# Kernel tuning notes

Measured on AMD Instinct MI355X. Metric: run time of the kernel, lower is better.

## Reference

```python
import jax, jax.numpy as jnp
import numpy as np

B, N1, N2, E = 8, 32, 32, 256
H = 8                 # num_heads == args.vir_heads
KD = E // H           # key dim per head = 32
HD = E // H           # head dim (value_dim == embed_dim)
L = N1 * N2           # 1024 tokens
SCALING = KD ** -0.5
LN_EPS = 1e-5


def _rel_pos_2d():
    # RetNetRelPosDeform2D with zero offsets (vir_use_deformable=False)
    half = 1.0 / 10000.0 ** jnp.linspace(0.0, 1.0, KD // 2)
    angle = jnp.repeat(half, 2)                                   # (KD,) interleaved pairs
    decay = jnp.log(1.0 - 2.0 ** (-2.0 - 5.0 * jnp.arange(H, dtype=jnp.float32) / H))  # (H,)
    i1 = jnp.arange(N1, dtype=jnp.float32)
    i2 = jnp.arange(N2, dtype=jnp.float32)
    index_k = (i1[:, None] + i2[None, :]).reshape(L)              # (L,)
    sin_k = jnp.sin(index_k[:, None] * angle[None, :])            # (L, KD)
    cos_k = jnp.cos(index_k[:, None] * angle[None, :])
    # zero offsets => index_q == index_k, broadcast over (B, H)
    sin_q = sin_k[None, None]                                     # (1,1,L,KD)
    cos_q = cos_k[None, None]
    # Manhattan distance decay mask on the 2D grid
    d = (jnp.abs(i1[:, None, None, None] - i1[None, None, :, None])
         + jnp.abs(i2[None, :, None, None] - i2[None, None, None, :])).reshape(L, L)
    mask = jnp.exp(d[None, :, :] * decay[:, None, None])          # (H, L, L)
    mask = jnp.nan_to_num(mask)
    mask = mask / jnp.sqrt(mask.sum(-1, keepdims=True))
    return sin_q, cos_q, sin_k, cos_k, mask


def rotate_every_two(x):
    x1 = x[..., ::2]
    x2 = x[..., 1::2]
    return jnp.stack((-x2, x1), axis=-1).reshape(x.shape)


def theta_shift(x, sin, cos):
    return x * cos + rotate_every_two(x) * sin


def setup_inputs() -> dict:
    key = jax.random.key(0)
    ks = jax.random.split(key, 5)
    gain_qkv = 2.0 ** -2.5 * (6.0 / (E + E)) ** 0.5  # xavier_uniform bound scale
    gain_o = 2.0 ** -1 * (6.0 / (E + E)) ** 0.5
    x = jax.random.normal(ks[0], (B, N1, N2, E), dtype=jnp.float32)
    Wq = jax.random.uniform(ks[1], (E, E), jnp.float32, -gain_qkv, gain_qkv)
    Wk = jax.random.uniform(ks[2], (E, E), jnp.float32, -gain_qkv, gain_qkv)
    Wv = jax.random.uniform(ks[3], (E, E), jnp.float32, -gain_qkv, gain_qkv)
    Wo = jax.random.uniform(ks[4], (E, E), jnp.float32, -gain_o, gain_o)
    ln_g = jnp.ones((HD,), jnp.float32)
    ln_b = jnp.zeros((HD,), jnp.float32)
    return {"x": x, "Wq": Wq, "Wk": Wk, "Wv": Wv, "Wo": Wo, "ln_g": ln_g, "ln_b": ln_b}


def reference(x, Wq, Wk, Wv, Wo, ln_g, ln_b):
    sin_q, cos_q, sin_k, cos_k, mask = _rel_pos_2d()
    xf = x.reshape(B, L, E)
    q = (xf @ Wq.T).reshape(B, L, H, KD).transpose(0, 2, 1, 3)    # (B,H,L,KD)
    k = (xf @ Wk.T * SCALING).reshape(B, L, H, KD).transpose(0, 2, 1, 3)
    vr = (xf @ Wv.T).reshape(B, L, H, HD).transpose(0, 2, 1, 3)   # (B,H,L,HD)
    qr = theta_shift(q, sin_q, cos_q)
    kr = theta_shift(k, sin_k[None, None], cos_k[None, None])
    qk = jnp.einsum('bhqd,bhkd->bhqk', qr, kr) * mask[None]       # (B,H,L,L)
    den = jnp.clip(jax.lax.stop_gradient(jnp.abs(qk)).sum(-1, keepdims=True), 1.0, 5e4)
    qk = qk / den
    out = jnp.einsum('bhqk,bhkd->bhqd', qk, vr).transpose(0, 2, 1, 3)  # (B,L,H,HD)
    mu = out.mean(-1, keepdims=True)
    var = out.var(-1, keepdims=True)
    out = (out - mu) / jnp.sqrt(var + LN_EPS) * ln_g + ln_b       # per-head LayerNorm
    out = jax.nn.gelu(out.reshape(B, L, H * HD), approximate=False)
    out = out @ Wo.T
    return out.reshape(B, N1, N2, E)
```

## Files before the change

### kernel.cpp

```cpp
#include <hip/hip_runtime.h>
#include <math.h>

typedef unsigned short u16;
typedef unsigned int u32;
typedef __bf16 bf16x8 __attribute__((ext_vector_type(8)));
typedef float f32x4 __attribute__((ext_vector_type(4)));

#define SCALING 0.17677669529663687f
#define LOG2E 1.44269504088896f
#define LOG2_10000 13.287712379549449f

__device__ __forceinline__ u16 f2bf(float f) {
    u32 u; __builtin_memcpy(&u, &f, 4);
    u = u + 0x7FFFu + ((u >> 16) & 1u);
    return (u16)(u >> 16);
}
__device__ __forceinline__ f32x4 mfma16(bf16x8 a, bf16x8 b, f32x4 c) {
    return __builtin_amdgcn_mfma_f32_16x16x32_bf16(a, b, c, 0, 0, 0);
}
__device__ __forceinline__ float decay_l2(int h) {
    return logf(1.0f - exp2f(-2.0f - 0.625f * (float)h)) * LOG2E;
}

__global__ __launch_bounds__(256) void cvt_kernel(
    const float* __restrict__ x,
    const float* __restrict__ Wq, const float* __restrict__ Wk,
    const float* __restrict__ Wv, const float* __restrict__ Wo,
    u16* __restrict__ xb, u16* __restrict__ wb) {
    int bid = blockIdx.x;
    const float* src; u16* dst; int off;
    if (bid < 1024) { src = x; dst = xb; off = bid * 2048; }
    else {
        int wsel = (bid - 1024) >> 5;
        src = (wsel == 0) ? Wq : (wsel == 1) ? Wk : (wsel == 2) ? Wv : Wo;
        dst = wb + wsel * 65536;
        off = ((bid - 1024) & 31) * 2048;
    }
    int i = off + threadIdx.x * 8;
    float4 a = *(const float4*)&src[i];
    float4 b = *(const float4*)&src[i + 4];
    union { int4 v; u16 s[8]; } t;
    t.s[0] = f2bf(a.x); t.s[1] = f2bf(a.y); t.s[2] = f2bf(a.z); t.s[3] = f2bf(a.w);
    t.s[4] = f2bf(b.x); t.s[5] = f2bf(b.y); t.s[6] = f2bf(b.z); t.s[7] = f2bf(b.w);
    *(int4*)&dst[i] = t.v;
}

__global__ __launch_bounds__(256) void gemm_bt_kernel(
    const u16* __restrict__ A, const u16* __restrict__ Wb,
    u16* __restrict__ O0, u16* __restrict__ O1, u16* __restrict__ O2,
    float* __restrict__ Of, int mode_base) {
    __shared__ u16 As[64 * 136];
    __shared__ u16 Ws[64 * 136];
    int z = blockIdx.z;
    const u16* W = Wb + z * 65536;
    u16* O = (z == 0) ? O0 : (z == 1) ? O1 : O2;
    int mode = mode_base + z;
    int n0 = blockIdx.x * 64, r0 = blockIdx.y * 64;
    int tid = threadIdx.x;
    int w = tid >> 6, lane = tid & 63, ln = lane & 15, quad = lane >> 4;
    f32x4 acc[4] = {};
#pragma unroll
    for (int ch = 0; ch < 2; ch++) {
        int k0 = ch * 128;
        if (ch) __syncthreads();
#pragma unroll
        for (int i = 0; i < 4; i++) {
            int c = tid + i * 256;
            int row = c >> 4, seg = c & 15;
            *(int4*)&As[row * 136 + seg * 8] = *(const int4*)&A[(long)(r0 + row) * 256 + k0 + seg * 8];
            *(int4*)&Ws[row * 136 + seg * 8] = *(const int4*)&W[(long)(n0 + row) * 256 + k0 + seg * 8];
        }
        __syncthreads();
#pragma unroll
        for (int kt = 0; kt < 4; kt++) {
            bf16x8 a = *(const bf16x8*)&As[(w * 16 + ln) * 136 + kt * 32 + quad * 8];
#pragma unroll
            for (int nt = 0; nt < 4; nt++) {
                bf16x8 b = *(const bf16x8*)&Ws[(nt * 16 + ln) * 136 + kt * 32 + quad * 8];
                acc[nt] = mfma16(a, b, acc[nt]);
            }
        }
    }
    int rowg = r0 + w * 16 + quad * 4;
    if (mode == 3) {
#pragma unroll
        for (int nt = 0; nt < 4; nt++) {
            int e = n0 + nt * 16 + ln;
#pragma unroll
            for (int r = 0; r < 4; r++)
                Of[(long)(rowg + r) * 256 + e] = acc[nt][r];
        }
        return;
    }
    float scl = (mode == 1) ? SCALING : 1.0f;
#pragma unroll
    for (int nt = 0; nt < 4; nt++) {
        int e = n0 + nt * 16 + ln;
        int d = e & 31, hh = e >> 5;
        float ang = exp2f(-LOG2_10000 * (1.0f / 15.0f) * (float)(d >> 1));
#pragma unroll
        for (int r = 0; r < 4; r++) {
            int gi = rowg + r;
            int b = gi >> 10, l = gi & 1023;
            float v = acc[nt][r] * scl;
            float p = __shfl_xor(v, 1);
            float res;
            if (mode == 2) {
                res = v;
            } else {
                float idx = (float)((l >> 5) + (l & 31));
                float sv, cv;
                __sincosf(idx * ang, &sv, &cv);
                res = (d & 1) ? (v * cv + p * sv) : (v * cv - p * sv);
            }
            O[(((long)(b * 8 + hh)) * 1024 + l) * 32 + d] = f2bf(res);
        }
    }
}

__global__ __launch_bounds__(256) void attn_kernel(
    const u16* __restrict__ qr, const u16* __restrict__ kr, const u16* __restrict__ vr,
    const float* __restrict__ lng, const float* __restrict__ lnb,
    u16* __restrict__ out) {
    __shared__ u16 Qs[64 * 40];
    __shared__ u16 Ks[64 * 40];
    __shared__ u16 Vt[32 * 72];
    __shared__ u16 Ps[64 * 72];
    __shared__ float Tt[64];
    __shared__ float Ss[32];
    __shared__ float rq[64];
    int b = blockIdx.z, h = blockIdx.y, q0 = blockIdx.x * 64;
    int tid = threadIdx.x, w = tid >> 6, lane = tid & 63, ln = lane & 15, quad = lane >> 4;
    long bh = b * 8 + h;
    const u16* qb = qr + bh * 32768;
    const u16* kb = kr + bh * 32768;
    const u16* vb = vr + bh * 32768;
    float dec = decay_l2(h);
    {
        int row = tid >> 2, seg = tid & 3;
        *(int4*)&Qs[row * 40 + seg * 8] = *(const int4*)&qb[(q0 + row) * 32 + seg * 8];
        if (tid < 63) Tt[tid] = exp2f(dec * (float)tid);
    }
    __syncthreads();
    if (tid < 32) {
        float s = 0.0f;
#pragma unroll
        for (int b2 = 0; b2 < 32; b2++) s += Tt[abs(tid - b2)];
        Ss[tid] = s;
    }
    __syncthreads();
    if (tid < 64) {
        int q = q0 + tid;
        rq[tid] = rsqrtf(Ss[q >> 5] * Ss[q & 31]);
    }
    __syncthreads();
    int m0 = w * 16;
    bf16x8 aq = *(const bf16x8*)&Qs[(m0 + ln) * 40 + quad * 8];
    int q1r[4], q2r[4]; float rqv[4];
#pragma unroll
    for (int r = 0; r < 4; r++) {
        int qrow = m0 + quad * 4 + r;
        int q = q0 + qrow;
        q1r[r] = q >> 5; q2r[r] = q & 31;
        rqv[r] = rq[qrow];
    }
    f32x4 accO[2] = {};
    float den[4] = {0.f, 0.f, 0.f, 0.f};
    for (int kt = 0; kt < 16; kt++) {
        int k0 = kt * 64;
        {
            int row = tid >> 2, seg = tid & 3;
            *(int4*)&Ks[row * 40 + seg * 8] = *(const int4*)&kb[(k0 + row) * 32 + seg * 8];
            union { int4 v; u16 s[8]; } vv;
            vv.v = *(const int4*)&vb[(k0 + row) * 32 + seg * 8];
#pragma unroll
            for (int i = 0; i < 8; i++) Vt[(seg * 8 + i) * 72 + row] = vv.s[i];
        }
        __syncthreads();
        f32x4 zero = {};
#pragma unroll
        for (int nt = 0; nt < 4; nt++) {
            bf16x8 bk = *(const bf16x8*)&Ks[(nt * 16 + ln) * 40 + quad * 8];
            f32x4 s = mfma16(aq, bk, zero);
            int col = nt * 16 + ln;
            int k = k0 + col, k1 = k >> 5, k2 = k & 31;
#pragma unroll
            for (int r = 0; r < 4; r++) {
                int d = abs(q1r[r] - k1) + abs(q2r[r] - k2);
                float m = Tt[d] * rqv[r];
                float p = s[r] * m;
                den[r] += fabsf(p);
                Ps[(m0 + quad * 4 + r) * 72 + col] = f2bf(p);
            }
        }
#pragma unroll
        for (int c2 = 0; c2 < 2; c2++) {
            bf16x8 ap = *(const bf16x8*)&Ps[(m0 + ln) * 72 + c2 * 32 + quad * 8];
#pragma unroll
            for (int nv = 0; nv < 2; nv++) {
                bf16x8 bv = *(const bf16x8*)&Vt[(nv * 16 + ln) * 72 + c2 * 32 + quad * 8];
                accO[nv] = mfma16(ap, bv, accO[nv]);
            }
        }
        __syncthreads();
    }
#pragma unroll
    for (int m = 1; m < 16; m <<= 1)
#pragma unroll
        for (int r = 0; r < 4; r++) den[r] += __shfl_xor(den[r], m);
    float o[2][4], s1[4], s2[4];
#pragma unroll
    for (int r = 0; r < 4; r++) {
        float id = 1.0f / fminf(fmaxf(den[r], 1.0f), 50000.0f);
        o[0][r] = accO[0][r] * id;
        o[1][r] = accO[1][r] * id;
        s1[r] = o[0][r] + o[1][r];
        s2[r] = o[0][r] * o[0][r] + o[1][r] * o[1][r];
    }
#pragma unroll
    for (int m = 1; m < 16; m <<= 1)
#pragma unroll
        for (int r = 0; r < 4; r++) {
            s1[r] += __shfl_xor(s1[r], m);
            s2[r] += __shfl_xor(s2[r], m);
        }
    float g[2] = {lng[ln], lng[16 + ln]};
    float bb[2] = {lnb[ln], lnb[16 + ln]};
#pragma unroll
    for (int r = 0; r < 4; r++) {
        float mean = s1[r] * (1.0f / 32.0f);
        float var = s2[r] * (1.0f / 32.0f) - mean * mean;
        float rstd = rsqrtf(var + 1e-5f);
        int l = q0 + m0 + quad * 4 + r;
#pragma unroll
        for (int nv = 0; nv < 2; nv++) {
            float x = (o[nv][r] - mean) * rstd * g[nv] + bb[nv];
            float ge = 0.5f * x * (1.0f + erff(x * 0.70710678118654752f));
            out[((long)(b * 1024 + l)) * 256 + h * 32 + nv * 16 + ln] = f2bf(ge);
        }
    }
}

extern "C" void kernel_launch(void* const* d_in, const int* in_sizes, int n_in,
                              void* d_out, int out_size, void* d_ws, size_t ws_size,
                              hipStream_t stream) {
    const float* x   = (const float*)d_in[0];
    const float* Wq  = (const float*)d_in[1];
    const float* Wk  = (const float*)d_in[2];
    const float* Wv  = (const float*)d_in[3];
    const float* Wo  = (const float*)d_in[4];
    const float* lng = (const float*)d_in[5];
    const float* lnb = (const float*)d_in[6];
    float* outp = (float*)d_out;

    u16* xb   = (u16*)d_ws;
    u16* wb   = xb + 2097152;
    u16* qr   = wb + 262144;
    u16* kr   = qr + 2097152;
    u16* vr   = kr + 2097152;
    u16* attn = vr + 2097152;

    cvt_kernel<<<1152, 256, 0, stream>>>(x, Wq, Wk, Wv, Wo, xb, wb);
    gemm_bt_kernel<<<dim3(4, 128, 3), 256, 0, stream>>>(xb, wb, qr, kr, vr, nullptr, 0);
    attn_kernel<<<dim3(16, 8, 8), 256, 0, stream>>>(qr, kr, vr, lng, lnb, attn);
    gemm_bt_kernel<<<dim3(4, 128, 1), 256, 0, stream>>>(attn, wb + 3 * 65536, nullptr, nullptr, nullptr, outp, 3);
}
```

Before: 128.9 us.

## Double-buffer K/V tiles, transpose MFMA roles, and factor decay mask in attention

```diff
diff --git a/kernel.cpp b/kernel.cpp
--- a/kernel.cpp
+++ b/kernel.cpp
@@ -14,6 +14,12 @@
     u32 u; __builtin_memcpy(&u, &f, 4);
     u = u + 0x7FFFu + ((u >> 16) & 1u);
     return (u16)(u >> 16);
+}
+__device__ __forceinline__ u32 fbits(float f) {
+    u32 u; __builtin_memcpy(&u, &f, 4); return u;
+}
+__device__ __forceinline__ u32 pack_bf16(float lo, float hi) {
+    return __builtin_amdgcn_perm(fbits(hi) + 0x8000u, fbits(lo) + 0x8000u, 0x07060302u);
 }
 __device__ __forceinline__ f32x4 mfma16(bf16x8 a, bf16x8 b, f32x4 c) {
     return __builtin_amdgcn_mfma_f32_16x16x32_bf16(a, b, c, 0, 0, 0);
@@ -49,8 +55,8 @@
     const u16* __restrict__ A, const u16* __restrict__ Wb,
     u16* __restrict__ O0, u16* __restrict__ O1, u16* __restrict__ O2,
     float* __restrict__ Of, int mode_base) {
-    __shared__ u16 As[64 * 136];
-    __shared__ u16 Ws[64 * 136];
+    __shared__ __align__(16) u16 As[64 * 136];
+    __shared__ __align__(16) u16 Ws[64 * 136];
     int z = blockIdx.z;
     const u16* W = Wb + z * 65536;
     u16* O = (z == 0) ? O0 : (z == 1) ? O1 : O2;
@@ -122,13 +128,13 @@
     const u16* __restrict__ qr, const u16* __restrict__ kr, const u16* __restrict__ vr,
     const float* __restrict__ lng, const float* __restrict__ lnb,
     u16* __restrict__ out) {
-    __shared__ u16 Qs[64 * 40];
-    __shared__ u16 Ks[64 * 40];
-    __shared__ u16 Vt[32 * 72];
-    __shared__ u16 Ps[64 * 72];
+    __shared__ __align__(16) u16 Qs[64 * 40];
+    __shared__ __align__(16) u16 Ks[2][64 * 40];
+    __shared__ __align__(16) u32 VtW[2][32 * 36];
+    __shared__ __align__(16) u32 PsW[4][16 * 36];
     __shared__ float Tt[64];
     __shared__ float Ss[32];
-    __shared__ float rq[64];
+    __shared__ float lngS[32], lnbS[32];
     int b = blockIdx.z, h = blockIdx.y, q0 = blockIdx.x * 64;
     int tid = threadIdx.x, w = tid >> 6, lane = tid & 63, ln = lane & 15, quad = lane >> 4;
     long bh = b * 8 + h;
@@ -139,8 +145,14 @@
     {
         int row = tid >> 2, seg = tid & 3;
         *(int4*)&Qs[row * 40 + seg * 8] = *(const int4*)&qb[(q0 + row) * 32 + seg * 8];
-        if (tid < 63) Tt[tid] = exp2f(dec * (float)tid);
-    }
+    }
+    if (tid < 63) Tt[tid] = exp2f(dec * (float)tid);
+    if (tid >= 64 && tid < 96) { lngS[tid - 64] = lng[tid - 64]; lnbS[tid - 64] = lnb[tid - 64]; }
+    int krow = tid >> 2, kseg = tid & 3;
+    int vp = tid >> 3, vseg = tid & 7;
+    int4 kreg = *(const int4*)&kb[(long)krow * 32 + kseg * 8];
+    int2 v0 = *(const int2*)&vb[(long)(vp * 2) * 32 + vseg * 4];
+    int2 v1 = *(const int2*)&vb[(long)(vp * 2 + 1) * 32 + vseg * 4];
     __syncthreads();
     if (tid < 32) {
         float s = 0.0f;
@@ -148,97 +160,102 @@
         for (int b2 = 0; b2 < 32; b2++) s += Tt[abs(tid - b2)];
         Ss[tid] = s;
     }
+    *(int4*)&Ks[0][krow * 40 + kseg * 8] = kreg;
+    VtW[0][(vseg * 4 + 0) * 36 + vp] = __builtin_amdgcn_perm(v1.x, v0.x, 0x05040100u);
+    VtW[0][(vseg * 4 + 1) * 36 + vp] = __builtin_amdgcn_perm(v1.x, v0.x, 0x07060302u);
+    VtW[0][(vseg * 4 + 2) * 36 + vp] = __builtin_amdgcn_perm(v1.y, v0.y, 0x05040100u);
+    VtW[0][(vseg * 4 + 3) * 36 + vp] = __builtin_amdgcn_perm(v1.y, v0.y, 0x07060302u);
+    kreg = *(const int4*)&kb[(long)(64 + krow) * 32 + kseg * 8];
+    v0 = *(const int2*)&vb[(long)(64 + vp * 2) * 32 + vseg * 4];
+    v1 = *(const int2*)&vb[(long)(64 + vp * 2 + 1) * 32 + vseg * 4];
     __syncthreads();
-    if (tid < 64) {
-        int q = q0 + tid;
-        rq[tid] = rsqrtf(Ss[q >> 5] * Ss[q & 31]);
-    }
-    __syncthreads();
-    int m0 = w * 16;
-    bf16x8 aq = *(const bf16x8*)&Qs[(m0 + ln) * 40 + quad * 8];
-    int q1r[4], q2r[4]; float rqv[4];
-#pragma unroll
-    for (int r = 0; r < 4; r++) {
-        int qrow = m0 + quad * 4 + r;
-        int q = q0 + qrow;
-        q1r[r] = q >> 5; q2r[r] = q & 31;
-        rqv[r] = rq[qrow];
-    }
-    f32x4 accO[2] = {};
-    float den[4] = {0.f, 0.f, 0.f, 0.f};
+    int q = q0 + w * 16 + ln;
+    int q1i = q >> 5, q2i = q & 31;
+    float rqv = rsqrtf(Ss[q1i] * Ss[q2i]);
+    bf16x8 aq = *(const bf16x8*)&Qs[(w * 16 + ln) * 40 + quad * 8];
+    float bt[2][4];
+#pragma unroll
+    for (int s2 = 0; s2 < 2; s2++)
+#pragma unroll
+        for (int r = 0; r < 4; r++)
+            bt[s2][r] = Tt[abs(q2i - (s2 * 16 + quad * 4 + r))];
+    f32x4 accO0 = {}, accO1 = {};
+    float den = 0.0f;
+    u32* psw = &PsW[w][0];
     for (int kt = 0; kt < 16; kt++) {
-        int k0 = kt * 64;
-        {
-            int row = tid >> 2, seg = tid & 3;
-            *(int4*)&Ks[row * 40 + seg * 8] = *(const int4*)&kb[(k0 + row) * 32 + seg * 8];
-            union { int4 v; u16 s[8]; } vv;
-            vv.v = *(const int4*)&vb[(k0 + row) * 32 + seg * 8];
-#pragma unroll
-            for (int i = 0; i < 8; i++) Vt[(seg * 8 + i) * 72 + row] = vv.s[i];
-        }
-        __syncthreads();
-        f32x4 zero = {};
+        int cur = kt & 1;
+        float a0 = Tt[abs(q1i - 2 * kt)] * rqv;
+        float a1 = Tt[abs(q1i - 2 * kt - 1)] * rqv;
+        const u16* ksb = &Ks[cur][0];
+        const u32* vtb = &VtW[cur][0];
 #pragma unroll
         for (int nt = 0; nt < 4; nt++) {
-            bf16x8 bk = *(const bf16x8*)&Ks[(nt * 16 + ln) * 40 + quad * 8];
-            f32x4 s = mfma16(aq, bk, zero);
-            int col = nt * 16 + ln;
-            int k = k0 + col, k1 = k >> 5, k2 = k & 31;
-#pragma unroll
-            for (int r = 0; r < 4; r++) {
-                int d = abs(q1r[r] - k1) + abs(q2r[r] - k2);
-                float m = Tt[d] * rqv[r];
-                float p = s[r] * m;
-                den[r] += fabsf(p);
-                Ps[(m0 + quad * 4 + r) * 72 + col] = f2bf(p);
+            bf16x8 ak = *(const bf16x8*)&ksb[(nt * 16 + ln) * 40 + quad * 8];
+            f32x4 s = mfma16(ak, aq, (f32x4){0.f, 0.f, 0.f, 0.f});
+            float aa = (nt & 2) ? a1 : a0;
+            float p0 = s[0] * aa * bt[nt & 1][0];
+            float p1 = s[1] * aa * bt[nt & 1][1];
+            float p2 = s[2] * aa * bt[nt & 1][2];
+            float p3 = s[3] * aa * bt[nt & 1][3];
+            den += fabsf(p0); den += fabsf(p1); den += fabsf(p2); den += fabsf(p3);
+            int2 pw;
+            pw.x = (int)pack_bf16(p0, p1);
+            pw.y = (int)pack_bf16(p2, p3);
+            *(int2*)&psw[ln * 36 + nt * 8 + quad * 2] = pw;
+        }
+#pragma unroll
+        for (int c = 0; c < 2; c++) {
+            bf16x8 bp  = *(const bf16x8*)&psw[ln * 36 + c * 16 + quad * 4];
+            bf16x8 av0 = *(const bf16x8*)&vtb[(ln)      * 36 + c * 16 + quad * 4];
+            bf16x8 av1 = *(const bf16x8*)&vtb[(16 + ln) * 36 + c * 16 + quad * 4];
+            accO0 = mfma16(av0, bp, accO0);
+            accO1 = mfma16(av1, bp, accO1);
+        }
+        if (kt < 15) {
+            int nb = 1 - cur;
+            *(int4*)&Ks[nb][krow * 40 + kseg * 8] = kreg;
+            VtW[nb][(vseg * 4 + 0) * 36 + vp] = __builtin_amdgcn_perm(v1.x, v0.x, 0x05040100u);
+            VtW[nb][(vseg * 4 + 1) * 36 + vp] = __builtin_amdgcn_perm(v1.x, v0.x, 0x07060302u);
+            VtW[nb][(vseg * 4 + 2) * 36 + vp] = __builtin_amdgcn_perm(v1.y, v0.y, 0x05040100u);
+            VtW[nb][(vseg * 4 + 3) * 36 + vp] = __builtin_amdgcn_perm(v1.y, v0.y, 0x07060302u);
+            if (kt < 14) {
+                int t2 = (kt + 2) * 64;
+                kreg = *(const int4*)&kb[(long)(t2 + krow) * 32 + kseg * 8];
+                v0 = *(const int2*)&vb[(long)(t2 + vp * 2) * 32 + vseg * 4];
+                v1 = *(const int2*)&vb[(long)(t2 + vp * 2 + 1) * 32 + vseg * 4];
             }
-        }
-#pragma unroll
-        for (int c2 = 0; c2 < 2; c2++) {
-            bf16x8 ap = *(const bf16x8*)&Ps[(m0 + ln) * 72 + c2 * 32 + quad * 8];
-#pragma unroll
-            for (int nv = 0; nv < 2; nv++) {
-                bf16x8 bv = *(const bf16x8*)&Vt[(nv * 16 + ln) * 72 + c2 * 32 + quad * 8];
-                accO[nv] = mfma16(ap, bv, accO[nv]);
-            }
-        }
-        __syncthreads();
-    }
-#pragma unroll
-    for (int m = 1; m < 16; m <<= 1)
-#pragma unroll
-        for (int r = 0; r < 4; r++) den[r] += __shfl_xor(den[r], m);
-    float o[2][4], s1[4], s2[4];
-#pragma unroll
-    for (int r = 0; r < 4; r++) {
-        float id = 1.0f / fminf(fmaxf(den[r], 1.0f), 50000.0f);
-        o[0][r] = accO[0][r] * id;
-        o[1][r] = accO[1][r] * id;
-        s1[r] = o[0][r] + o[1][r];
-        s2[r] = o[0][r] * o[0][r] + o[1][r] * o[1][r];
-    }
-#pragma unroll
-    for (int m = 1; m < 16; m <<= 1)
+            __syncthreads();
+        }
+    }
+    den += __shfl_xor(den, 16);
+    den += __shfl_xor(den, 32);
+    float id = 1.0f / fminf(fmaxf(den, 1.0f), 50000.0f);
+    float o[8];
+#pragma unroll
+    for (int r = 0; r < 4; r++) { o[r] = accO0[r] * id; o[4 + r] = accO1[r] * id; }
+    float s1 = 0.0f, s2 = 0.0f;
+#pragma unroll
+    for (int i = 0; i < 8; i++) { s1 += o[i]; s2 += o[i] * o[i]; }
+    s1 += __shfl_xor(s1, 16); s1 += __shfl_xor(s1, 32);
+    s2 += __shfl_xor(s2, 16); s2 += __shfl_xor(s2, 32);
+    float mean = s1 * (1.0f / 32.0f);
+    float var = s2 * (1.0f / 32.0f) - mean * mean;
+    float rstd = rsqrtf(var + 1e-5f);
+    float xg[8];
+#pragma unroll
+    for (int nv = 0; nv < 2; nv++)
 #pragma unroll
         for (int r = 0; r < 4; r++) {
-            s1[r] += __shfl_xor(s1[r], m);
-            s2[r] += __shfl_xor(s2[r], m);
-        }
-    float g[2] = {lng[ln], lng[16 + ln]};
-    float bb[2] = {lnb[ln], lnb[16 + ln]};
-#pragma unroll
-    for (int r = 0; r < 4; r++) {
-        float mean = s1[r] * (1.0f / 32.0f);
-        float var = s2[r] * (1.0f / 32.0f) - mean * mean;
-        float rstd = rsqrtf(var + 1e-5f);
-        int l = q0 + m0 + quad * 4 + r;
-#pragma unroll
-        for (int nv = 0; nv < 2; nv++) {
-            float x = (o[nv][r] - mean) * rstd * g[nv] + bb[nv];
-            float ge = 0.5f * x * (1.0f + erff(x * 0.70710678118654752f));
-            out[((long)(b * 1024 + l)) * 256 + h * 32 + nv * 16 + ln] = f2bf(ge);
-        }
-    }
+            int d = nv * 16 + quad * 4 + r;
+            float xv = (o[nv * 4 + r] - mean) * rstd * lngS[d] + lnbS[d];
+            xg[nv * 4 + r] = 0.5f * xv * (1.0f + erff(xv * 0.70710678118654752f));
+        }
+    u16* orow = out + ((long)(b * 1024 + q)) * 256 + h * 32;
+    int2 st0, st1;
+    st0.x = (int)pack_bf16(xg[0], xg[1]); st0.y = (int)pack_bf16(xg[2], xg[3]);
+    st1.x = (int)pack_bf16(xg[4], xg[5]); st1.y = (int)pack_bf16(xg[6], xg[7]);
+    *(int2*)&orow[quad * 4] = st0;
+    *(int2*)&orow[16 + quad * 4] = st1;
 }
 
 extern "C" void kernel_launch(void* const* d_in, const int* in_sizes, int n_in,
```

Result: faster. 114.8 us (-10.9%).
